# Performance work log

Hardware: AMD Instinct MI355X
Metric: run time of the kernel (lower is better)

The kernel has to match this reference:

```python
import math
import jax, jax.numpy as jnp
import numpy as np

B, T, N, F, H = 8, 16, 64, 64, 1024  # feature_dim must equal num_regions for the einsum to be valid


def _linear_init(key, out_dim, in_dim):
    kw, kb = jax.random.split(key)
    s = 1.0 / np.sqrt(in_dim)
    W = jax.random.uniform(kw, (out_dim, in_dim), jnp.float32, -s, s)
    b = jax.random.uniform(kb, (out_dim,), jnp.float32, -s, s)
    return W, b


def setup_inputs() -> dict:
    key = jax.random.key(0)
    k0, k1, k2, k3, k4 = jax.random.split(key, 5)
    M = jax.random.normal(k0, (B, T, N, N, F), jnp.float32)
    Wo, bo = _linear_init(k1, H, N * F)      # origin_proj
    Wso, bso = _linear_init(k2, N, H)        # origin_score
    Wd, bd = _linear_init(k3, H, N * F)      # dest_proj
    Wsd, bsd = _linear_init(k4, N, H)        # dest_score
    return {"M": M, "Wo": Wo, "bo": bo, "Wso": Wso, "bso": bso,
            "Wd": Wd, "bd": bd, "Wsd": Wsd, "bsd": bsd}


def _sparse_attention(scores, u):
    # scores: (BT, N, N)
    p = jax.nn.softmax(scores, axis=-1)
    entropy = -jnp.sum(p * jnp.log(p + 1e-9), axis=-1)          # (BT, N)
    _, top_idx = jax.lax.top_k(-entropy, u)                      # u smallest-entropy rows
    bt = entropy.shape[0]
    mask = jnp.zeros(entropy.shape, bool).at[jnp.arange(bt)[:, None], top_idx].set(True)
    return p * mask[..., None]                                   # zero all but u rows


def reference(M, Wo, bo, Wso, bso, Wd, bd, Wsd, bsd):
    Bb, Tt, Nn, _, Ff = M.shape
    BT = Bb * Tt
    X = M.reshape(BT, Nn, Nn * Ff)                               # origin view
    Y = jnp.transpose(M, (0, 1, 3, 2, 4)).reshape(BT, Nn, Nn * Ff)  # dest view
    omega_scores = (X @ Wo.T + bo) @ Wso.T + bso                 # (BT, N, N)
    delta_scores = (Y @ Wd.T + bd) @ Wsd.T + bsd                 # (BT, N, N)
    u = max(1, int(math.log(Nn)))
    omega = _sparse_attention(omega_scores, u)
    delta = _sparse_attention(delta_scores, u)
    M_flat = M.reshape(BT, Nn, Nn, Ff)
    out = jnp.einsum('bij,bjkl->bikl', omega, M_flat)            # (BT, N, N, F)
    out = jnp.einsum('bikl,bjl->bijk', out, delta)               # requires F == N
    return out.reshape(Bb, Tt, Nn, Nn, Ff)
```

## Files before the change

### kernel.cpp

```cpp
#include <hip/hip_runtime.h>
#include <math.h>

#define NB 8
#define NT 16
#define NN 64
#define NF 64
#define NH 1024
#define BT 128
#define NFK 4096

typedef float  f32x4 __attribute__((ext_vector_type(4)));
typedef short  s16x8 __attribute__((ext_vector_type(8)));

#define MFMA_B16(a, b, c) __builtin_amdgcn_mfma_f32_16x16x32_bf16(a, b, c, 0, 0, 0)

#define WFRAG_USHORTS 1048576
#define BEFF_FOFF     524288
#define PSEL_FOFF     524416
#define IDX_FOFF      589952

__device__ __forceinline__ void split_bf16(float v, unsigned short& hi, unsigned short& lo) {
    unsigned u = __float_as_uint(v);
    float r = v - __uint_as_float(u & 0xFFFF0000u);
    hi = (unsigned short)(u >> 16);
    lo = (unsigned short)(__float_as_uint(r) >> 16);
}

__device__ __forceinline__ void split8(const float4& a0, const float4& a1, s16x8& ah, s16x8& al) {
    float fa[8];
    *(float4*)&fa[0] = a0; *(float4*)&fa[4] = a1;
    #pragma unroll
    for (int j = 0; j < 8; ++j) {
        unsigned u = __float_as_uint(fa[j]);
        float r = fa[j] - __uint_as_float(u & 0xFFFF0000u);
        ah[j] = (short)(u >> 16);
        al[j] = (short)(__float_as_uint(r) >> 16);
    }
}

__global__ __launch_bounds__(256) void fold_kernel(
    const float* __restrict__ Wso, const float* __restrict__ Wo,
    const float* __restrict__ Wsd, const float* __restrict__ Wd,
    unsigned short* __restrict__ wfrag)
{
    const int which = blockIdx.y;
    const float* __restrict__ A  = which ? Wsd : Wso;
    const float* __restrict__ Bm = which ? Wd  : Wo;
    const int c0 = blockIdx.x * 64;

    __shared__ float As[64][68];
    __shared__ float Bs[64][68];

    const int t  = threadIdx.x;
    const int tx = t & 15, ty = t >> 4;

    float acc[4][4] = {};

    for (int h0 = 0; h0 < NH; h0 += 64) {
        #pragma unroll
        for (int it = 0; it < 4; ++it) {
            int r = (t >> 4) + it * 16, c4 = (t & 15) * 4;
            *(float4*)&As[r][c4] = *(const float4*)&A[r * NH + h0 + c4];
        }
        #pragma unroll
        for (int it = 0; it < 4; ++it) {
            int h = (t >> 4) + it * 16, c4 = (t & 15) * 4;
            float4 v = *(const float4*)&Bm[(size_t)(h0 + h) * NFK + c0 + c4];
            Bs[c4 + 0][h] = v.x; Bs[c4 + 1][h] = v.y;
            Bs[c4 + 2][h] = v.z; Bs[c4 + 3][h] = v.w;
        }
        __syncthreads();
        #pragma unroll 4
        for (int kk = 0; kk < 64; kk += 4) {
            float4 a4[4], b4[4];
            #pragma unroll
            for (int m = 0; m < 4; ++m) a4[m] = *(const float4*)&As[ty + 16 * m][kk];
            #pragma unroll
            for (int n = 0; n < 4; ++n) b4[n] = *(const float4*)&Bs[tx + 16 * n][kk];
            #pragma unroll
            for (int m = 0; m < 4; ++m)
                #pragma unroll
                for (int n = 0; n < 4; ++n)
                    acc[m][n] += a4[m].x * b4[n].x + a4[m].y * b4[n].y
                               + a4[m].z * b4[n].z + a4[m].w * b4[n].w;
        }
        __syncthreads();
    }
    #pragma unroll
    for (int m = 0; m < 4; ++m)
        #pragma unroll
        for (int n = 0; n < 4; ++n) {
            int r = ty + 16 * m;
            int c = c0 + tx + 16 * n;
            unsigned short hi, lo;
            split_bf16(acc[m][n], hi, lo);
            int ct = r >> 4, lane = (((c >> 3) & 3) << 4) | (r & 15);
            int ks = c >> 5, j = c & 7;
            size_t offh = ((((size_t)(which * 2 + 0) * 4 + ct) * 128 + ks) * 64 + lane) * 8 + j;
            size_t offl = ((((size_t)(which * 2 + 1) * 4 + ct) * 128 + ks) * 64 + lane) * 8 + j;
            wfrag[offh] = hi;
            wfrag[offl] = lo;
        }
}

__global__ __launch_bounds__(256) void bias_kernel(
    const float* __restrict__ Wso, const float* __restrict__ bo, const float* __restrict__ bso,
    const float* __restrict__ Wsd, const float* __restrict__ bd, const float* __restrict__ bsd,
    float* __restrict__ beff)
{
    const int which = blockIdx.x;
    const float* __restrict__ Ws = which ? Wsd : Wso;
    const float* __restrict__ bb = which ? bd  : bo;
    const float* __restrict__ bs = which ? bsd : bso;
    const int t = threadIdx.x;
    const int r = t >> 2, c = t & 3;
    const float* wp = Ws + r * NH + c * 256;
    const float* bp = bb + c * 256;
    float s = 0.f;
    #pragma unroll 4
    for (int i = 0; i < 64; ++i) {
        float4 wv = *(const float4*)(wp + 4 * i);
        float4 bv = *(const float4*)(bp + 4 * i);
        s += wv.x * bv.x + wv.y * bv.y + wv.z * bv.z + wv.w * bv.w;
    }
    __shared__ float part[64][4];
    part[r][c] = s;
    __syncthreads();
    if (t < 64)
        beff[which * 64 + t] = bs[t] + part[t][0] + part[t][1] + part[t][2] + part[t][3];
}

__global__ __launch_bounds__(256) void scores_mfma(
    const float* __restrict__ M, const unsigned short* __restrict__ wfrag,
    const float* __restrict__ beff,
    float* __restrict__ psel, int* __restrict__ idxsel)
{
    const int bt = blockIdx.x, which = blockIdx.y;
    const float* __restrict__ Mbt = M + (size_t)bt * NN * NN * NF;
    const int t = threadIdx.x;
    const int w = t >> 6, l = t & 63, q = l >> 4, ln = l & 15;
    const int arow = 16 * w + ln;

    const unsigned short* __restrict__ wfl = wfrag + (size_t)which * WFRAG_USHORTS / 2 + (size_t)l * 8;
#define BOFF(part, ct, ks) ((((part) * 4 + (ct)) * 128 + (ks)) * 512)

#define AADDR(ks) (Mbt + q * 8 + ((which == 0) \
        ? (arow * NFK + (ks) * 32) \
        : ((((ks) >> 1) * NFK) + arow * 64 + (((ks) & 1) * 32))))

    f32x4 acc[4];
    #pragma unroll
    for (int ct = 0; ct < 4; ++ct) acc[ct] = (f32x4)0.f;

    float4 Ac[4][2], An[4][2];
    #pragma unroll
    for (int kk = 0; kk < 4; ++kk) {
        const float* ap = AADDR(kk);
        Ac[kk][0] = *(const float4*)ap;
        Ac[kk][1] = *(const float4*)(ap + 4);
    }
    s16x8 bhc[4], blc[4];
    #pragma unroll
    for (int ct = 0; ct < 4; ++ct) {
        bhc[ct] = *(const s16x8*)(wfl + BOFF(0, ct, 0));
        blc[ct] = *(const s16x8*)(wfl + BOFF(1, ct, 0));
    }

    for (int g = 0; g < 32; ++g) {
        if (g + 1 < 32) {
            #pragma unroll
            for (int kk = 0; kk < 4; ++kk) {
                const float* ap = AADDR(4 * (g + 1) + kk);
                An[kk][0] = *(const float4*)ap;
                An[kk][1] = *(const float4*)(ap + 4);
            }
        }
        #pragma unroll
        for (int kk = 0; kk < 4; ++kk) {
            const int ks = 4 * g + kk;
            s16x8 bhn[4], bln[4];
            if (ks + 1 < 128) {
                #pragma unroll
                for (int ct = 0; ct < 4; ++ct) {
                    bhn[ct] = *(const s16x8*)(wfl + BOFF(0, ct, ks + 1));
                    bln[ct] = *(const s16x8*)(wfl + BOFF(1, ct, ks + 1));
                }
            }
            s16x8 ah, al;
            split8(Ac[kk][0], Ac[kk][1], ah, al);
            #pragma unroll
            for (int ct = 0; ct < 4; ++ct) {
                acc[ct] = MFMA_B16(ah, bhc[ct], acc[ct]);
                acc[ct] = MFMA_B16(al, bhc[ct], acc[ct]);
                acc[ct] = MFMA_B16(ah, blc[ct], acc[ct]);
            }
            if (ks + 1 < 128) {
                #pragma unroll
                for (int ct = 0; ct < 4; ++ct) { bhc[ct] = bhn[ct]; blc[ct] = bln[ct]; }
            }
        }
        #pragma unroll
        for (int kk = 0; kk < 4; ++kk) { Ac[kk][0] = An[kk][0]; Ac[kk][1] = An[kk][1]; }
    }
#undef AADDR
#undef BOFF

    float bv[4];
    #pragma unroll
    for (int ct = 0; ct < 4; ++ct) bv[ct] = beff[which * 64 + 16 * ct + ln];

    float p[4][4];
    float H[4];
    #pragma unroll
    for (int reg = 0; reg < 4; ++reg) {
        float s0 = acc[0][reg] + bv[0], s1 = acc[1][reg] + bv[1];
        float s2 = acc[2][reg] + bv[2], s3 = acc[3][reg] + bv[3];
        float m = fmaxf(fmaxf(s0, s1), fmaxf(s2, s3));
        #pragma unroll
        for (int msk = 1; msk < 16; msk <<= 1) m = fmaxf(m, __shfl_xor(m, msk));
        float e0 = expf(s0 - m), e1 = expf(s1 - m), e2 = expf(s2 - m), e3 = expf(s3 - m);
        float sum = e0 + e1 + e2 + e3;
        #pragma unroll
        for (int msk = 1; msk < 16; msk <<= 1) sum += __shfl_xor(sum, msk);
        float inv = 1.0f / sum;
        float pp0 = e0 * inv, pp1 = e1 * inv, pp2 = e2 * inv, pp3 = e3 * inv;
        p[0][reg] = pp0; p[1][reg] = pp1; p[2][reg] = pp2; p[3][reg] = pp3;
        float h = pp0 * logf(pp0 + 1e-9f) + pp1 * logf(pp1 + 1e-9f)
                + pp2 * logf(pp2 + 1e-9f) + pp3 * logf(pp3 + 1e-9f);
        #pragma unroll
        for (int msk = 1; msk < 16; msk <<= 1) h += __shfl_xor(h, msk);
        H[reg] = -h;
    }

    __shared__ float ent[64];
    __shared__ int sel[4];
    if (ln == 0) {
        #pragma unroll
        for (int reg = 0; reg < 4; ++reg) ent[16 * w + 4 * q + reg] = H[reg];
    }
    __syncthreads();
    if (t == 0) {
        unsigned long long used = 0ull;
        for (int s = 0; s < 4; ++s) {
            float best = INFINITY; int bi = 0;
            for (int r = 0; r < 64; ++r) {
                if ((used >> r) & 1ull) continue;
                if (ent[r] < best) { best = ent[r]; bi = r; }
            }
            used |= 1ull << bi;
            sel[s] = bi;
        }
    }
    __syncthreads();
    if (t < 4) idxsel[((size_t)which * BT + bt) * 4 + t] = sel[t];
    #pragma unroll
    for (int s = 0; s < 4; ++s) {
        int row = sel[s];
        if (w == (row >> 4) && q == ((row >> 2) & 3)) {
            int reg = row & 3;
            #pragma unroll
            for (int ct = 0; ct < 4; ++ct)
                psel[(((size_t)which * BT + bt) * 4 + s) * 64 + 16 * ct + ln] = p[ct][reg];
        }
    }
}

__global__ __launch_bounds__(256) void scatter_kernel(
    const float* __restrict__ M, const float* __restrict__ psel,
    const int* __restrict__ idxsel, float* __restrict__ out)
{
    const int bt = blockIdx.x, kc = blockIdx.y;
    __shared__ float po[4][64], pd[4][64];
    __shared__ int io[4], id[4];
    __shared__ int rio[64], rid[64];
    __shared__ float o1[4][16][68];
    __shared__ float res[4][4][16];

    const int t = threadIdx.x;
    {
        int s = t >> 6, l = t & 63;
        po[s][l] = psel[(((size_t)0 * BT + bt) * 4 + s) * 64 + l];
        pd[s][l] = psel[(((size_t)1 * BT + bt) * 4 + s) * 64 + l];
    }
    if (t < 64) { rio[t] = -1; rid[t] = -1; }
    if (t >= 64 && t < 68) {
        int s = t - 64;
        io[s] = idxsel[((size_t)0 * BT + bt) * 4 + s];
        id[s] = idxsel[((size_t)1 * BT + bt) * 4 + s];
    }
    __syncthreads();
    if (t < 4) { rio[io[t]] = t; rid[id[t]] = t; }

    const float* __restrict__ Ms = M + (size_t)bt * NN * NFK + kc * 1024 + t * 4;

    float4 a0 = {0,0,0,0}, a1 = {0,0,0,0}, a2 = {0,0,0,0}, a3 = {0,0,0,0};
    #pragma unroll 4
    for (int j = 0; j < NN; ++j) {
        float4 mv = *(const float4*)(Ms + (size_t)j * NFK);
        float w0 = po[0][j], w1 = po[1][j], w2 = po[2][j], w3 = po[3][j];
        a0.x += w0 * mv.x; a0.y += w0 * mv.y; a0.z += w0 * mv.z; a0.w += w0 * mv.w;
        a1.x += w1 * mv.x; a1.y += w1 * mv.y; a1.z += w1 * mv.z; a1.w += w1 * mv.w;
        a2.x += w2 * mv.x; a2.y += w2 * mv.y; a2.z += w2 * mv.z; a2.w += w2 * mv.w;
        a3.x += w3 * mv.x; a3.y += w3 * mv.y; a3.z += w3 * mv.z; a3.w += w3 * mv.w;
    }
    {
        int kl = t >> 4, l4 = (t & 15) * 4;
        *(float4*)&o1[0][kl][l4] = a0;
        *(float4*)&o1[1][kl][l4] = a1;
        *(float4*)&o1[2][kl][l4] = a2;
        *(float4*)&o1[3][kl][l4] = a3;
    }
    __syncthreads();
    {
        int i = t >> 6, jj = (t >> 4) & 3, k = t & 15;
        float v = 0.f;
        #pragma unroll
        for (int l4 = 0; l4 < 16; ++l4) {
            float4 ov = *(const float4*)&o1[i][k][l4 * 4];
            float4 pv = *(const float4*)&pd[jj][l4 * 4];
            v += ov.x * pv.x + ov.y * pv.y + ov.z * pv.z + ov.w * pv.w;
        }
        res[i][jj][k] = v;
    }
    __syncthreads();

    float* __restrict__ obase = out + (size_t)bt * NN * NN * NN + kc * 16;
    #pragma unroll 4
    for (int c = 0; c < 16; ++c) {
        int pos = t + 256 * c;
        int i = pos >> 6, jj = pos & 63;
        int ii = rio[i], jd = rid[jj];
        float* dst = obase + (size_t)pos * 64;
        if (ii >= 0 && jd >= 0) {
            *(float4*)(dst + 0)  = *(const float4*)&res[ii][jd][0];
            *(float4*)(dst + 4)  = *(const float4*)&res[ii][jd][4];
            *(float4*)(dst + 8)  = *(const float4*)&res[ii][jd][8];
            *(float4*)(dst + 12) = *(const float4*)&res[ii][jd][12];
        } else {
            float4 z = {0,0,0,0};
            *(float4*)(dst + 0)  = z;
            *(float4*)(dst + 4)  = z;
            *(float4*)(dst + 8)  = z;
            *(float4*)(dst + 12) = z;
        }
    }
}

extern "C" void kernel_launch(void* const* d_in, const int* in_sizes, int n_in,
                              void* d_out, int out_size, void* d_ws, size_t ws_size,
                              hipStream_t stream)
{
    const float* M   = (const float*)d_in[0];
    const float* Wo  = (const float*)d_in[1];
    const float* bo  = (const float*)d_in[2];
    const float* Wso = (const float*)d_in[3];
    const float* bso = (const float*)d_in[4];
    const float* Wd  = (const float*)d_in[5];
    const float* bd  = (const float*)d_in[6];
    const float* Wsd = (const float*)d_in[7];
    const float* bsd = (const float*)d_in[8];
    float* out = (float*)d_out;

    unsigned short* wfrag = (unsigned short*)d_ws;
    float* beff = (float*)d_ws + BEFF_FOFF;
    float* psel = (float*)d_ws + PSEL_FOFF;
    int*   idxs = (int*)((float*)d_ws + IDX_FOFF);

    fold_kernel<<<dim3(64, 2), 256, 0, stream>>>(Wso, Wo, Wsd, Wd, wfrag);
    bias_kernel<<<2, 256, 0, stream>>>(Wso, bo, bso, Wsd, bd, bsd, beff);
    scores_mfma<<<dim3(BT, 2), 256, 0, stream>>>(M, wfrag, beff, psel, idxs);
    scatter_kernel<<<dim3(BT, 4), 256, 0, stream>>>(M, psel, idxs, out);
}
```

Before: 444.1 us.

## Split-K fold and score GEMMs across more blocks, separate output writer

The weight-fold GEMM now uses narrower column tiles and splits the hidden dimension into chunks, and a separate reduce kernel packs the results into bf16 fragments. The score MFMA kernel splits K into four chunks that write fp32 partials, and a new finalize kernel sums them and does the softmax, entropy and top-k. The scatter stage becomes a small compute kernel plus a wide writer kernel with one block per output row. The aim is to fill many more CUs than the 128-256 block grids did, at the cost of extra workspace traffic for partials and more kernel launches.

Result: faster. 405.7 us (-8.7%).

```diff
diff --git a/kernel.cpp b/kernel.cpp
--- a/kernel.cpp
+++ b/kernel.cpp
@@ -14,10 +14,11 @@
 
 #define MFMA_B16(a, b, c) __builtin_amdgcn_mfma_f32_16x16x32_bf16(a, b, c, 0, 0, 0)
 
-#define WFRAG_USHORTS 1048576
-#define BEFF_FOFF     524288
-#define PSEL_FOFF     524416
-#define IDX_FOFF      589952
+#define BEFF_FOFF   524288
+#define PSEL_FOFF   524416
+#define RTAB_FOFF   589952
+#define RES_FOFF    606336
+#define DYN_FOFF    737408
 
 __device__ __forceinline__ void split_bf16(float v, unsigned short& hi, unsigned short& lo) {
     unsigned u = __float_as_uint(v);
@@ -38,47 +39,48 @@
     }
 }
 
-__global__ __launch_bounds__(256) void fold_kernel(
+__global__ __launch_bounds__(256) void fold_part(
     const float* __restrict__ Wso, const float* __restrict__ Wo,
     const float* __restrict__ Wsd, const float* __restrict__ Wd,
-    unsigned short* __restrict__ wfrag)
-{
-    const int which = blockIdx.y;
+    float* __restrict__ fpart, int hchunk)
+{
+    const int which = blockIdx.y, kc = blockIdx.z;
     const float* __restrict__ A  = which ? Wsd : Wso;
     const float* __restrict__ Bm = which ? Wd  : Wo;
-    const int c0 = blockIdx.x * 64;
+    const int c0 = blockIdx.x * 32;
 
     __shared__ float As[64][68];
-    __shared__ float Bs[64][68];
-
-    const int t  = threadIdx.x;
-    const int tx = t & 15, ty = t >> 4;
-
-    float acc[4][4] = {};
-
-    for (int h0 = 0; h0 < NH; h0 += 64) {
+    __shared__ float Bs[32][68];
+
+    const int t = threadIdx.x;
+    const int tx = t & 7, ty = t >> 3;
+
+    float acc[2][4] = {};
+
+    const int h0beg = kc * hchunk, h0end = h0beg + hchunk;
+    for (int h0 = h0beg; h0 < h0end; h0 += 64) {
         #pragma unroll
         for (int it = 0; it < 4; ++it) {
             int r = (t >> 4) + it * 16, c4 = (t & 15) * 4;
             *(float4*)&As[r][c4] = *(const float4*)&A[r * NH + h0 + c4];
         }
         #pragma unroll
-        for (int it = 0; it < 4; ++it) {
-            int h = (t >> 4) + it * 16, c4 = (t & 15) * 4;
-            float4 v = *(const float4*)&Bm[(size_t)(h0 + h) * NFK + c0 + c4];
-            Bs[c4 + 0][h] = v.x; Bs[c4 + 1][h] = v.y;
-            Bs[c4 + 2][h] = v.z; Bs[c4 + 3][h] = v.w;
+        for (int it = 0; it < 2; ++it) {
+            int h = (t >> 3) + it * 32, cq = t & 7;
+            float4 v = *(const float4*)&Bm[(size_t)(h0 + h) * NFK + c0 + cq * 4];
+            Bs[cq * 4 + 0][h] = v.x; Bs[cq * 4 + 1][h] = v.y;
+            Bs[cq * 4 + 2][h] = v.z; Bs[cq * 4 + 3][h] = v.w;
         }
         __syncthreads();
         #pragma unroll 4
         for (int kk = 0; kk < 64; kk += 4) {
-            float4 a4[4], b4[4];
+            float4 a4[2], b4[4];
+            a4[0] = *(const float4*)&As[ty][kk];
+            a4[1] = *(const float4*)&As[ty + 32][kk];
             #pragma unroll
-            for (int m = 0; m < 4; ++m) a4[m] = *(const float4*)&As[ty + 16 * m][kk];
+            for (int n = 0; n < 4; ++n) b4[n] = *(const float4*)&Bs[tx + 8 * n][kk];
             #pragma unroll
-            for (int n = 0; n < 4; ++n) b4[n] = *(const float4*)&Bs[tx + 16 * n][kk];
-            #pragma unroll
-            for (int m = 0; m < 4; ++m)
+            for (int m = 0; m < 2; ++m)
                 #pragma unroll
                 for (int n = 0; n < 4; ++n)
                     acc[m][n] += a4[m].x * b4[n].x + a4[m].y * b4[n].y
@@ -86,21 +88,45 @@
         }
         __syncthreads();
     }
-    #pragma unroll
-    for (int m = 0; m < 4; ++m)
-        #pragma unroll
-        for (int n = 0; n < 4; ++n) {
-            int r = ty + 16 * m;
-            int c = c0 + tx + 16 * n;
-            unsigned short hi, lo;
-            split_bf16(acc[m][n], hi, lo);
-            int ct = r >> 4, lane = (((c >> 3) & 3) << 4) | (r & 15);
-            int ks = c >> 5, j = c & 7;
-            size_t offh = ((((size_t)(which * 2 + 0) * 4 + ct) * 128 + ks) * 64 + lane) * 8 + j;
-            size_t offl = ((((size_t)(which * 2 + 1) * 4 + ct) * 128 + ks) * 64 + lane) * 8 + j;
-            wfrag[offh] = hi;
-            wfrag[offl] = lo;
-        }
+    float* __restrict__ outp = fpart + ((size_t)(kc * 2 + which) * 64) * NFK;
+    #pragma unroll
+    for (int m = 0; m < 2; ++m)
+        #pragma unroll
+        for (int n = 0; n < 4; ++n)
+            outp[(size_t)(ty + 32 * m) * NFK + c0 + tx + 8 * n] = acc[m][n];
+}
+
+__global__ __launch_bounds__(256) void fold_reduce(
+    const float* __restrict__ fpart, unsigned short* __restrict__ wfrag, int fcc)
+{
+    const int which = blockIdx.y;
+    const int c0 = blockIdx.x * 64;
+    const int t = threadIdx.x;
+    const int r = t >> 2, cb = (t & 3) * 16;
+
+    float s[16] = {};
+    for (int c = 0; c < fcc; ++c) {
+        const float* __restrict__ p =
+            fpart + ((size_t)(c * 2 + which) * 64 + r) * NFK + c0 + cb;
+        #pragma unroll
+        for (int qq = 0; qq < 4; ++qq) {
+            float4 v = *(const float4*)(p + 4 * qq);
+            s[4 * qq + 0] += v.x; s[4 * qq + 1] += v.y;
+            s[4 * qq + 2] += v.z; s[4 * qq + 3] += v.w;
+        }
+    }
+    #pragma unroll
+    for (int jj = 0; jj < 16; ++jj) {
+        int c = c0 + cb + jj;
+        unsigned short hi, lo;
+        split_bf16(s[jj], hi, lo);
+        int ct = r >> 4, lane = (((c >> 3) & 3) << 4) | (r & 15);
+        int ks = c >> 5, j = c & 7;
+        size_t offh = ((((size_t)(which * 2 + 0) * 4 + ct) * 128 + ks) * 64 + lane) * 8 + j;
+        size_t offl = ((((size_t)(which * 2 + 1) * 4 + ct) * 128 + ks) * 64 + lane) * 8 + j;
+        wfrag[offh] = hi;
+        wfrag[offl] = lo;
+    }
 }
 
 __global__ __launch_bounds__(256) void bias_kernel(
@@ -130,24 +156,25 @@
         beff[which * 64 + t] = bs[t] + part[t][0] + part[t][1] + part[t][2] + part[t][3];
 }
 
-__global__ __launch_bounds__(256) void scores_mfma(
+__global__ __launch_bounds__(256) void scores_part(
     const float* __restrict__ M, const unsigned short* __restrict__ wfrag,
-    const float* __restrict__ beff,
-    float* __restrict__ psel, int* __restrict__ idxsel)
-{
-    const int bt = blockIdx.x, which = blockIdx.y;
+    float* __restrict__ spart, int ksc)
+{
+    const int bt = blockIdx.x, which = blockIdx.y, kc = blockIdx.z;
     const float* __restrict__ Mbt = M + (size_t)bt * NN * NN * NF;
     const int t = threadIdx.x;
     const int w = t >> 6, l = t & 63, q = l >> 4, ln = l & 15;
     const int arow = 16 * w + ln;
 
-    const unsigned short* __restrict__ wfl = wfrag + (size_t)which * WFRAG_USHORTS / 2 + (size_t)l * 8;
+    const unsigned short* __restrict__ wfl = wfrag + (size_t)which * 524288 + (size_t)l * 8;
 #define BOFF(part, ct, ks) ((((part) * 4 + (ct)) * 128 + (ks)) * 512)
-
 #define AADDR(ks) (Mbt + q * 8 + ((which == 0) \
         ? (arow * NFK + (ks) * 32) \
         : ((((ks) >> 1) * NFK) + arow * 64 + (((ks) & 1) * 32))))
 
+    const int ks0 = kc * ksc, ksend = ks0 + ksc;
+    const int g0 = ks0 >> 2, gend = ksend >> 2;
+
     f32x4 acc[4];
     #pragma unroll
     for (int ct = 0; ct < 4; ++ct) acc[ct] = (f32x4)0.f;
@@ -155,19 +182,19 @@
     float4 Ac[4][2], An[4][2];
     #pragma unroll
     for (int kk = 0; kk < 4; ++kk) {
-        const float* ap = AADDR(kk);
+        const float* ap = AADDR(ks0 + kk);
         Ac[kk][0] = *(const float4*)ap;
         Ac[kk][1] = *(const float4*)(ap + 4);
     }
     s16x8 bhc[4], blc[4];
     #pragma unroll
     for (int ct = 0; ct < 4; ++ct) {
-        bhc[ct] = *(const s16x8*)(wfl + BOFF(0, ct, 0));
-        blc[ct] = *(const s16x8*)(wfl + BOFF(1, ct, 0));
-    }
-
-    for (int g = 0; g < 32; ++g) {
-        if (g + 1 < 32) {
+        bhc[ct] = *(const s16x8*)(wfl + BOFF(0, ct, ks0));
+        blc[ct] = *(const s16x8*)(wfl + BOFF(1, ct, ks0));
+    }
+
+    for (int g = g0; g < gend; ++g) {
+        if (g + 1 < gend) {
             #pragma unroll
             for (int kk = 0; kk < 4; ++kk) {
                 const float* ap = AADDR(4 * (g + 1) + kk);
@@ -179,7 +206,8 @@
         for (int kk = 0; kk < 4; ++kk) {
             const int ks = 4 * g + kk;
             s16x8 bhn[4], bln[4];
-            if (ks + 1 < 128) {
+            const bool pf = (ks + 1 < ksend);
+            if (pf) {
                 #pragma unroll
                 for (int ct = 0; ct < 4; ++ct) {
                     bhn[ct] = *(const s16x8*)(wfl + BOFF(0, ct, ks + 1));
@@ -194,7 +222,7 @@
                 acc[ct] = MFMA_B16(al, bhc[ct], acc[ct]);
                 acc[ct] = MFMA_B16(ah, blc[ct], acc[ct]);
             }
-            if (ks + 1 < 128) {
+            if (pf) {
                 #pragma unroll
                 for (int ct = 0; ct < 4; ++ct) { bhc[ct] = bhn[ct]; blc[ct] = bln[ct]; }
             }
@@ -205,91 +233,107 @@
 #undef AADDR
 #undef BOFF
 
-    float bv[4];
-    #pragma unroll
-    for (int ct = 0; ct < 4; ++ct) bv[ct] = beff[which * 64 + 16 * ct + ln];
-
-    float p[4][4];
-    float H[4];
-    #pragma unroll
-    for (int reg = 0; reg < 4; ++reg) {
-        float s0 = acc[0][reg] + bv[0], s1 = acc[1][reg] + bv[1];
-        float s2 = acc[2][reg] + bv[2], s3 = acc[3][reg] + bv[3];
-        float m = fmaxf(fmaxf(s0, s1), fmaxf(s2, s3));
-        #pragma unroll
-        for (int msk = 1; msk < 16; msk <<= 1) m = fmaxf(m, __shfl_xor(m, msk));
-        float e0 = expf(s0 - m), e1 = expf(s1 - m), e2 = expf(s2 - m), e3 = expf(s3 - m);
-        float sum = e0 + e1 + e2 + e3;
-        #pragma unroll
-        for (int msk = 1; msk < 16; msk <<= 1) sum += __shfl_xor(sum, msk);
-        float inv = 1.0f / sum;
-        float pp0 = e0 * inv, pp1 = e1 * inv, pp2 = e2 * inv, pp3 = e3 * inv;
-        p[0][reg] = pp0; p[1][reg] = pp1; p[2][reg] = pp2; p[3][reg] = pp3;
-        float h = pp0 * logf(pp0 + 1e-9f) + pp1 * logf(pp1 + 1e-9f)
-                + pp2 * logf(pp2 + 1e-9f) + pp3 * logf(pp3 + 1e-9f);
-        #pragma unroll
-        for (int msk = 1; msk < 16; msk <<= 1) h += __shfl_xor(h, msk);
-        H[reg] = -h;
-    }
+    float* __restrict__ pout = spart + ((size_t)(kc * 2 + which) * BT + bt) * 4096;
+    #pragma unroll
+    for (int ct = 0; ct < 4; ++ct)
+        #pragma unroll
+        for (int reg = 0; reg < 4; ++reg)
+            pout[(16 * w + 4 * q + reg) * 64 + 16 * ct + ln] = acc[ct][reg];
+}
+
+__global__ __launch_bounds__(256) void finalize_kernel(
+    const float* __restrict__ spart, const float* __restrict__ beff,
+    float* __restrict__ psel, int* __restrict__ rtab, int scc)
+{
+    const int bt = blockIdx.x, which = blockIdx.y;
+    const int t = threadIdx.x;
+    const int row = t >> 2, cb = (t & 3) * 16;
+
+    float s[16] = {};
+    for (int c = 0; c < scc; ++c) {
+        const float* __restrict__ p =
+            spart + ((size_t)(c * 2 + which) * BT + bt) * 4096 + row * 64 + cb;
+        #pragma unroll
+        for (int qq = 0; qq < 4; ++qq) {
+            float4 v = *(const float4*)(p + 4 * qq);
+            s[4 * qq + 0] += v.x; s[4 * qq + 1] += v.y;
+            s[4 * qq + 2] += v.z; s[4 * qq + 3] += v.w;
+        }
+    }
+    #pragma unroll
+    for (int jj = 0; jj < 16; ++jj) s[jj] += beff[which * 64 + cb + jj];
+
+    float m = -INFINITY;
+    #pragma unroll
+    for (int jj = 0; jj < 16; ++jj) m = fmaxf(m, s[jj]);
+    m = fmaxf(m, __shfl_xor(m, 1));
+    m = fmaxf(m, __shfl_xor(m, 2));
+
+    float e[16], sum = 0.f;
+    #pragma unroll
+    for (int jj = 0; jj < 16; ++jj) { e[jj] = expf(s[jj] - m); sum += e[jj]; }
+    sum += __shfl_xor(sum, 1);
+    sum += __shfl_xor(sum, 2);
+    const float inv = 1.0f / sum;
+
+    float pv[16], h = 0.f;
+    #pragma unroll
+    for (int jj = 0; jj < 16; ++jj) {
+        pv[jj] = e[jj] * inv;
+        h += pv[jj] * logf(pv[jj] + 1e-9f);
+    }
+    h += __shfl_xor(h, 1);
+    h += __shfl_xor(h, 2);
+    const float H = -h;
 
     __shared__ float ent[64];
     __shared__ int sel[4];
-    if (ln == 0) {
-        #pragma unroll
-        for (int reg = 0; reg < 4; ++reg) ent[16 * w + 4 * q + reg] = H[reg];
-    }
+    if ((t & 3) == 0) ent[row] = H;
     __syncthreads();
     if (t == 0) {
         unsigned long long used = 0ull;
-        for (int s = 0; s < 4; ++s) {
+        for (int ss = 0; ss < 4; ++ss) {
             float best = INFINITY; int bi = 0;
             for (int r = 0; r < 64; ++r) {
                 if ((used >> r) & 1ull) continue;
                 if (ent[r] < best) { best = ent[r]; bi = r; }
             }
             used |= 1ull << bi;
-            sel[s] = bi;
-        }
-    }
-    __syncthreads();
-    if (t < 4) idxsel[((size_t)which * BT + bt) * 4 + t] = sel[t];
-    #pragma unroll
-    for (int s = 0; s < 4; ++s) {
-        int row = sel[s];
-        if (w == (row >> 4) && q == ((row >> 2) & 3)) {
-            int reg = row & 3;
+            sel[ss] = bi;
+        }
+    }
+    __syncthreads();
+
+    int* __restrict__ rt = rtab + ((size_t)which * BT + bt) * 64;
+    if (t < 64) rt[t] = -1;
+    __syncthreads();
+    if (t < 4) rt[sel[t]] = t;
+
+    #pragma unroll
+    for (int ss = 0; ss < 4; ++ss) {
+        if (row == sel[ss]) {
+            float* __restrict__ dp = psel + (((size_t)which * BT + bt) * 4 + ss) * 64 + cb;
             #pragma unroll
-            for (int ct = 0; ct < 4; ++ct)
-                psel[(((size_t)which * BT + bt) * 4 + s) * 64 + 16 * ct + ln] = p[ct][reg];
-        }
-    }
-}
-
-__global__ __launch_bounds__(256) void scatter_kernel(
+            for (int jj = 0; jj < 16; ++jj) dp[jj] = pv[jj];
+        }
+    }
+}
+
+__global__ __launch_bounds__(256) void res_compute(
     const float* __restrict__ M, const float* __restrict__ psel,
-    const int* __restrict__ idxsel, float* __restrict__ out)
+    float* __restrict__ resb)
 {
     const int bt = blockIdx.x, kc = blockIdx.y;
     __shared__ float po[4][64], pd[4][64];
-    __shared__ int io[4], id[4];
-    __shared__ int rio[64], rid[64];
     __shared__ float o1[4][16][68];
-    __shared__ float res[4][4][16];
 
     const int t = threadIdx.x;
     {
-        int s = t >> 6, l = t & 63;
-        po[s][l] = psel[(((size_t)0 * BT + bt) * 4 + s) * 64 + l];
-        pd[s][l] = psel[(((size_t)1 * BT + bt) * 4 + s) * 64 + l];
-    }
-    if (t < 64) { rio[t] = -1; rid[t] = -1; }
-    if (t >= 64 && t < 68) {
-        int s = t - 64;
-        io[s] = idxsel[((size_t)0 * BT + bt) * 4 + s];
-        id[s] = idxsel[((size_t)1 * BT + bt) * 4 + s];
-    }
-    __syncthreads();
-    if (t < 4) { rio[io[t]] = t; rid[id[t]] = t; }
+        int ss = t >> 6, l = t & 63;
+        po[ss][l] = psel[(((size_t)0 * BT + bt) * 4 + ss) * 64 + l];
+        pd[ss][l] = psel[(((size_t)1 * BT + bt) * 4 + ss) * 64 + l];
+    }
+    __syncthreads();
 
     const float* __restrict__ Ms = M + (size_t)bt * NN * NFK + kc * 1024 + t * 4;
 
@@ -317,33 +361,40 @@
         #pragma unroll
         for (int l4 = 0; l4 < 16; ++l4) {
             float4 ov = *(const float4*)&o1[i][k][l4 * 4];
-            float4 pv = *(const float4*)&pd[jj][l4 * 4];
-            v += ov.x * pv.x + ov.y * pv.y + ov.z * pv.z + ov.w * pv.w;
-        }
-        res[i][jj][k] = v;
-    }
-    __syncthreads();
-
-    float* __restrict__ obase = out + (size_t)bt * NN * NN * NN + kc * 16;
-    #pragma unroll 4
-    for (int c = 0; c < 16; ++c) {
-        int pos = t + 256 * c;
-        int i = pos >> 6, jj = pos & 63;
-        int ii = rio[i], jd = rid[jj];
-        float* dst = obase + (size_t)pos * 64;
-        if (ii >= 0 && jd >= 0) {
-            *(float4*)(dst + 0)  = *(const float4*)&res[ii][jd][0];
-            *(float4*)(dst + 4)  = *(const float4*)&res[ii][jd][4];
-            *(float4*)(dst + 8)  = *(const float4*)&res[ii][jd][8];
-            *(float4*)(dst + 12) = *(const float4*)&res[ii][jd][12];
-        } else {
-            float4 z = {0,0,0,0};
-            *(float4*)(dst + 0)  = z;
-            *(float4*)(dst + 4)  = z;
-            *(float4*)(dst + 8)  = z;
-            *(float4*)(dst + 12) = z;
-        }
-    }
+            float4 pvv = *(const float4*)&pd[jj][l4 * 4];
+            v += ov.x * pvv.x + ov.y * pvv.y + ov.z * pvv.z + ov.w * pvv.w;
+        }
+        resb[(((size_t)bt * 4 + i) * 4 + jj) * 64 + kc * 16 + k] = v;
+    }
+}
+
+__global__ __launch_bounds__(256) void writer_kernel(
+    const float* __restrict__ resb, const int* __restrict__ rtab,
+    float* __restrict__ out)
+{
+    const int b = blockIdx.x, bt = b >> 6, i = b & 63;
+    const int t = threadIdx.x;
+    __shared__ float rl[4][64];
+
+    const int ii = rtab[((size_t)0 * BT + bt) * 64 + i];
+    const int jd = rtab[((size_t)1 * BT + bt) * 64 + (t >> 2)];
+    if (ii >= 0)
+        rl[t >> 6][t & 63] = resb[(((size_t)bt * 4 + ii) * 4 + (t >> 6)) * 64 + (t & 63)];
+    __syncthreads();
+
+    float4 v0 = {0,0,0,0}, v1 = {0,0,0,0}, v2 = {0,0,0,0}, v3 = {0,0,0,0};
+    if (ii >= 0 && jd >= 0) {
+        const int kb = (t & 3) * 16;
+        v0 = *(const float4*)&rl[jd][kb + 0];
+        v1 = *(const float4*)&rl[jd][kb + 4];
+        v2 = *(const float4*)&rl[jd][kb + 8];
+        v3 = *(const float4*)&rl[jd][kb + 12];
+    }
+    float* __restrict__ dst = out + (size_t)b * 4096 + t * 16;
+    *(float4*)(dst + 0)  = v0;
+    *(float4*)(dst + 4)  = v1;
+    *(float4*)(dst + 8)  = v2;
+    *(float4*)(dst + 12) = v3;
 }
 
 extern "C" void kernel_launch(void* const* d_in, const int* in_sizes, int n_in,
@@ -361,13 +412,26 @@
     const float* bsd = (const float*)d_in[8];
     float* out = (float*)d_out;
 
+    float* ws = (float*)d_ws;
     unsigned short* wfrag = (unsigned short*)d_ws;
-    float* beff = (float*)d_ws + BEFF_FOFF;
-    float* psel = (float*)d_ws + PSEL_FOFF;
-    int*   idxs = (int*)((float*)d_ws + IDX_FOFF);
-
-    fold_kernel<<<dim3(64, 2), 256, 0, stream>>>(Wso, Wo, Wsd, Wd, wfrag);
+    float* beff = ws + BEFF_FOFF;
+    float* psel = ws + PSEL_FOFF;
+    int*   rtab = (int*)(ws + RTAB_FOFF);
+    float* resb = ws + RES_FOFF;
+
+    int FCC = 2, SCC = 4;
+    {
+        size_t need = ((size_t)DYN_FOFF + (size_t)FCC * 524288 + (size_t)SCC * 1048576) * 4;
+        if (ws_size < need) { FCC = 1; SCC = 1; }
+    }
+    float* fpart = ws + DYN_FOFF;
+    float* spart = fpart + (size_t)FCC * 524288;
+
+    fold_part<<<dim3(128, 2, FCC), 256, 0, stream>>>(Wso, Wo, Wsd, Wd, fpart, NH / FCC);
     bias_kernel<<<2, 256, 0, stream>>>(Wso, bo, bso, Wsd, bd, bsd, beff);
-    scores_mfma<<<dim3(BT, 2), 256, 0, stream>>>(M, wfrag, beff, psel, idxs);
-    scatter_kernel<<<dim3(BT, 4), 256, 0, stream>>>(M, psel, idxs, out);
-}
+    fold_reduce<<<dim3(64, 2), 256, 0, stream>>>(fpart, wfrag, FCC);
+    scores_part<<<dim3(BT, 2, SCC), 256, 0, stream>>>(M, wfrag, spart, 128 / SCC);
+    finalize_kernel<<<dim3(BT, 2), 256, 0, stream>>>(spart, beff, psel, rtab, SCC);
+    res_compute<<<dim3(BT, 4), 256, 0, stream>>>(M, psel, resb);
+    writer_kernel<<<BT * 64, 256, 0, stream>>>(resb, rtab, out);
+}
```
